# Optimization experiments

Hardware: AMD Instinct MI355X
Metric: run time of the kernel (lower is better)

## Reference

```python
import jax, jax.numpy as jnp
import numpy as np
from functools import partial

B, T, H, W, CIN, F = 8, 16, 64, 64, 32, 32
K = 3
BN_EPS = 1e-3


def _conv(x, w):
    # x: [N,H,W,Cin], w: [kh,kw,Cin,Cout], SAME padding, stride 1
    return jax.lax.conv_general_dilated(
        x, w, window_strides=(1, 1), padding='SAME',
        dimension_numbers=('NHWC', 'HWIO', 'NHWC'))


def _hard_sigmoid(x):
    # Keras hard_sigmoid: clip(0.2*x + 0.5, 0, 1)
    return jnp.clip(0.2 * x + 0.5, 0.0, 1.0)


def setup_inputs() -> dict:
    key = jax.random.key(0)
    ks = jax.random.split(key, 4)
    x = jax.random.normal(ks[0], (B, T, H, W, CIN), dtype=jnp.float32)
    Wx = jax.random.normal(ks[1], (K, K, CIN, 4 * F), dtype=jnp.float32) * 0.05
    Wh = jax.random.normal(ks[2], (K, K, F, 4 * F), dtype=jnp.float32) * 0.05
    b = jnp.zeros((4 * F,), dtype=jnp.float32)
    gamma = jnp.ones((F,), dtype=jnp.float32)
    beta = jnp.zeros((F,), dtype=jnp.float32)
    moving_mean = jnp.zeros((F,), dtype=jnp.float32)
    moving_var = jnp.ones((F,), dtype=jnp.float32)
    return {"x": x, "Wx": Wx, "Wh": Wh, "b": b, "gamma": gamma,
            "beta": beta, "moving_mean": moving_mean, "moving_var": moving_var}


def _conv_lstm(x, Wx, Wh, b):
    # Precompute input-to-gate convs for all timesteps at once: [B*T,H,W,4F]
    xg = _conv(x.reshape(B * T, H, W, CIN), Wx) + b
    xg = xg.reshape(B, T, H, W, 4 * F).transpose(1, 0, 2, 3, 4)  # [T,B,H,W,4F]

    def step(carry, xg_t):
        h, c = carry
        g = xg_t + _conv(h, Wh)  # [B,H,W,4F]
        i, f, cc, o = jnp.split(g, 4, axis=-1)  # Keras gate order i,f,c,o
        i = _hard_sigmoid(i)
        f = _hard_sigmoid(f)
        o = _hard_sigmoid(o)
        c = f * c + i * jnp.tanh(cc)
        h = o * jnp.tanh(c)
        return (h, c), h

    h0 = jnp.zeros((B, H, W, F), dtype=x.dtype)
    c0 = jnp.zeros((B, H, W, F), dtype=x.dtype)
    _, hs = jax.lax.scan(step, (h0, c0), xg)  # hs: [T,B,H,W,F]
    return hs.transpose(1, 0, 2, 3, 4)  # [B,T,H,W,F]


def reference(x, Wx, Wh, b, gamma, beta, moving_mean, moving_var):
    y = _conv_lstm(x, Wx, Wh, b)
    # BatchNorm in inference mode (training=False): use moving stats, eps=1e-3
    inv = gamma * jax.lax.rsqrt(moving_var + BN_EPS)
    return y * inv + (beta - moving_mean * inv)
```

## Files before the change

### kernel.cpp

```cpp
#include <hip/hip_runtime.h>
#include <math.h>

#define PSTR 40
#define GSTR 35
#define GPL  (64 * GSTR)

typedef _Float16 half8 __attribute__((ext_vector_type(8)));
typedef float    f32x4 __attribute__((ext_vector_type(4)));

__device__ __forceinline__ float fast_tanh(float v) {
    float e = __expf(2.f * v);
    return 1.f - 2.f / (e + 1.f);
}
__device__ __forceinline__ float hsig(float v) {
    return fminf(fmaxf(0.2f * v + 0.5f, 0.f), 1.f);
}

__global__ void prep_w(const float* __restrict__ Wx, const float* __restrict__ Wh,
                       _Float16* __restrict__ Wcx, _Float16* __restrict__ Wch) {
    const int k = blockIdx.x;
    const int n = threadIdx.x;
    const int tap = k >> 6, ci = k & 63;
    if (ci < 32) Wcx[(tap * 128 + n) * 32 + ci]        = (_Float16)Wx[(tap * 32 + ci) * 128 + n];
    else         Wch[(tap * 128 + n) * 32 + (ci - 32)] = (_Float16)Wh[(tap * 32 + (ci - 32)) * 128 + n];
}

__global__ __launch_bounds__(256, 2)
void lstm_step_k(const float* __restrict__ x, const _Float16* __restrict__ Wcx,
                 const _Float16* __restrict__ Wch, const float* __restrict__ bias,
                 const float* __restrict__ gamma_, const float* __restrict__ beta_,
                 const float* __restrict__ mmean, const float* __restrict__ mvar,
                 const _Float16* __restrict__ hprev, _Float16* __restrict__ hnext,
                 float* __restrict__ csw, float* __restrict__ out, int t)
{
    __shared__ _Float16 xp[100 * PSTR];
    __shared__ _Float16 hp[100 * PSTR];
    __shared__ float    glds[4 * GPL];

    const int tid  = threadIdx.x;
    const int lane = tid & 63;
    const int w    = tid >> 6;
    const int l15  = lane & 15, quad = lane >> 4;
    const int b = blockIdx.x, tx = blockIdx.y, ty = blockIdx.z;
    const int px0 = tx * 8, py0 = ty * 8;
    const int tile = ty * 8 + tx;

    const float* xt = x + (((size_t)b * 16 + t) * 4096) * 32;
    for (int i = tid; i < 400; i += 256) {
        const int pos = i >> 2, q = i & 3;
        const int row = pos / 10, col = pos - row * 10;
        const int gy = py0 + row - 1, gx = px0 + col - 1;
        half8 hv = {0, 0, 0, 0, 0, 0, 0, 0};
        if ((unsigned)gy < 64u && (unsigned)gx < 64u) {
            const float* s = xt + ((size_t)(gy * 64 + gx)) * 32 + q * 8;
            const float4 v0 = *(const float4*)s;
            const float4 v1 = *(const float4*)(s + 4);
            hv = (half8){(_Float16)v0.x, (_Float16)v0.y, (_Float16)v0.z, (_Float16)v0.w,
                         (_Float16)v1.x, (_Float16)v1.y, (_Float16)v1.z, (_Float16)v1.w};
        }
        *(half8*)&xp[pos * PSTR + q * 8] = hv;
    }
    if (t > 0) {
        const _Float16* hb = hprev + (size_t)b * 4096 * 32;
        for (int i = tid; i < 400; i += 256) {
            const int pos = i >> 2, q = i & 3;
            const int row = pos / 10, col = pos - row * 10;
            const int gy = py0 + row - 1, gx = px0 + col - 1;
            half8 hv = {0, 0, 0, 0, 0, 0, 0, 0};
            if ((unsigned)gy < 64u && (unsigned)gx < 64u)
                hv = *(const half8*)(hb + ((size_t)(gy * 64 + gx)) * 32 + q * 8);
            *(half8*)&hp[pos * PSTR + q * 8] = hv;
        }
    }

    const float bi0 = bias[w * 32 + l15];
    const float bi1 = bias[w * 32 + 16 + l15];

    __syncthreads();

    f32x4 acc[4][2];
    #pragma unroll
    for (int mt = 0; mt < 4; ++mt) {
        acc[mt][0] = (f32x4){bi0, bi0, bi0, bi0};
        acc[mt][1] = (f32x4){bi1, bi1, bi1, bi1};
    }

    int pb[4];
    #pragma unroll
    for (int mt = 0; mt < 4; ++mt) {
        const int p = mt * 16 + l15;
        pb[mt] = ((mt * 2 + (l15 >> 3)) * 10 + (l15 & 7)) * PSTR + quad * 8;
    }
    const _Float16* wbx = Wcx + ((size_t)(w * 32 + l15)) * 32 + quad * 8;
    const _Float16* wbh = Wch + ((size_t)(w * 32 + l15)) * 32 + quad * 8;

    #pragma unroll
    for (int tap = 0; tap < 9; ++tap) {
        const int ky = tap / 3, kx = tap - ky * 3;
        const int toff = (ky * 10 + kx) * PSTR;
        half8 a[4];
        #pragma unroll
        for (int mt = 0; mt < 4; ++mt) a[mt] = *(const half8*)&xp[pb[mt] + toff];
        #pragma unroll
        for (int ntl = 0; ntl < 2; ++ntl) {
            const half8 bf = *(const half8*)(wbx + tap * 4096 + ntl * 512);
            #pragma unroll
            for (int mt = 0; mt < 4; ++mt)
                acc[mt][ntl] = __builtin_amdgcn_mfma_f32_16x16x32_f16(a[mt], bf, acc[mt][ntl], 0, 0, 0);
        }
    }
    if (t > 0) {
        #pragma unroll
        for (int tap = 0; tap < 9; ++tap) {
            const int ky = tap / 3, kx = tap - ky * 3;
            const int toff = (ky * 10 + kx) * PSTR;
            half8 a[4];
            #pragma unroll
            for (int mt = 0; mt < 4; ++mt) a[mt] = *(const half8*)&hp[pb[mt] + toff];
            #pragma unroll
            for (int ntl = 0; ntl < 2; ++ntl) {
                const half8 bf = *(const half8*)(wbh + tap * 4096 + ntl * 512);
                #pragma unroll
                for (int mt = 0; mt < 4; ++mt)
                    acc[mt][ntl] = __builtin_amdgcn_mfma_f32_16x16x32_f16(a[mt], bf, acc[mt][ntl], 0, 0, 0);
            }
        }
    }

    #pragma unroll
    for (int mt = 0; mt < 4; ++mt)
        #pragma unroll
        for (int ntl = 0; ntl < 2; ++ntl)
            #pragma unroll
            for (int r = 0; r < 4; ++r) {
                const int px = mt * 16 + quad * 4 + r;
                glds[w * GPL + px * GSTR + ntl * 16 + l15] = acc[mt][ntl][r];
            }

    __syncthreads();

    const int pxt = tid >> 2, f0 = (tid & 3) * 8;
    const int gy = py0 + (pxt >> 3), gx = px0 + (pxt & 7);

    float gav[8], bev[8], mmv[8], mvv[8];
    *(float4*)&gav[0] = *(const float4*)&gamma_[f0];
    *(float4*)&gav[4] = *(const float4*)&gamma_[f0 + 4];
    *(float4*)&bev[0] = *(const float4*)&beta_[f0];
    *(float4*)&bev[4] = *(const float4*)&beta_[f0 + 4];
    *(float4*)&mmv[0] = *(const float4*)&mmean[f0];
    *(float4*)&mmv[4] = *(const float4*)&mmean[f0 + 4];
    *(float4*)&mvv[0] = *(const float4*)&mvar[f0];
    *(float4*)&mvv[4] = *(const float4*)&mvar[f0 + 4];

    float* cp = csw + (((size_t)b * 64 + tile) * 256 + tid) * 8;
    float cov[8];
    #pragma unroll
    for (int j = 0; j < 8; ++j) cov[j] = 0.f;
    if (t > 0) {
        *(f32x4*)&cov[0] = *(const f32x4*)cp;
        *(f32x4*)&cov[4] = *(const f32x4*)(cp + 4);
    }

    const int gb = pxt * GSTR + f0;
    half8 hv8;
    float ov[8], cnv[8];
    #pragma unroll
    for (int j = 0; j < 8; ++j) {
        const float gi = glds[0 * GPL + gb + j];
        const float gf = glds[1 * GPL + gb + j];
        const float gc = glds[2 * GPL + gb + j];
        const float go = glds[3 * GPL + gb + j];
        const float inv = gav[j] * rsqrtf(mvv[j] + 1e-3f);
        const float bnb = bev[j] - mmv[j] * inv;
        const float cn = hsig(gf) * cov[j] + hsig(gi) * fast_tanh(gc);
        const float hh = hsig(go) * fast_tanh(cn);
        cnv[j] = cn;
        hv8[j] = (_Float16)hh;
        ov[j] = hh * inv + bnb;
    }

    const size_t pix = ((size_t)(gy * 64 + gx)) * 32 + f0;
    _Float16* hq = hnext + (size_t)b * 4096 * 32;
    float* oq = out + (((size_t)b * 16 + t) * 4096) * 32;
    *(half8*)(hq + pix) = hv8;
    *(float4*)(oq + pix)     = *(float4*)&ov[0];
    *(float4*)(oq + pix + 4) = *(float4*)&ov[4];
    *(f32x4*)cp       = *(f32x4*)&cnv[0];
    *(f32x4*)(cp + 4) = *(f32x4*)&cnv[4];
}

extern "C" void kernel_launch(void* const* d_in, const int* in_sizes, int n_in,
                              void* d_out, int out_size, void* d_ws, size_t ws_size,
                              hipStream_t stream)
{
    const float* x      = (const float*)d_in[0];
    const float* Wx     = (const float*)d_in[1];
    const float* Wh     = (const float*)d_in[2];
    const float* bias   = (const float*)d_in[3];
    const float* gamma_ = (const float*)d_in[4];
    const float* beta_  = (const float*)d_in[5];
    const float* mmean  = (const float*)d_in[6];
    const float* mvar   = (const float*)d_in[7];
    float* out = (float*)d_out;

    char* wsb = (char*)d_ws;
    _Float16* h0  = (_Float16*)(wsb);
    _Float16* h1  = (_Float16*)(wsb + (1 << 21));
    float*    csw = (float*)(wsb + (1 << 22));
    _Float16* Wcx = (_Float16*)(wsb + (1 << 23));
    _Float16* Wch = (_Float16*)(wsb + (1 << 23) + 73728);

    prep_w<<<dim3(576), dim3(128), 0, stream>>>(Wx, Wh, Wcx, Wch);

    _Float16* hpr = h0;
    _Float16* hnx = h1;
    for (int t = 0; t < 16; ++t) {
        lstm_step_k<<<dim3(8, 8, 8), 256, 0, stream>>>(
            x, Wcx, Wch, bias, gamma_, beta_, mmean, mvar, hpr, hnx, csw, out, t);
        _Float16* tmp = hpr; hpr = hnx; hnx = tmp;
    }
}
```

Baseline: 293.0 us.

## Halve spatial tile to 8x4 pixels, doubling grid blocks per LSTM step

Shrinks each block's output tile from 8x8 to 8x4 pixels, so the grid per timestep doubles to 1024 blocks. LDS use per block drops and launch bounds rise to 4 blocks per CU, which gives more parallelism and occupancy to hide the latency of each short step launch. It also drops the h and c stores on the last timestep and swaps the divide-by-10 for a multiply-shift. In exchange, the 3x3 halo now costs more redundant loads per output pixel, and each wave issues fewer MFMAs per weight fragment it loads.

```diff
diff --git a/kernel.cpp b/kernel.cpp
--- a/kernel.cpp
+++ b/kernel.cpp
@@ -1,11 +1,12 @@
 #include <hip/hip_runtime.h>
 #include <math.h>
 
-#define PSTR 40
-#define GSTR 35
-#define GPL  (64 * GSTR)
+#define PSTR  40
+#define GSTR  35
+#define GPL32 (32 * GSTR)
 
 typedef _Float16 half8 __attribute__((ext_vector_type(8)));
+typedef _Float16 half4 __attribute__((ext_vector_type(4)));
 typedef float    f32x4 __attribute__((ext_vector_type(4)));
 
 __device__ __forceinline__ float fast_tanh(float v) {
@@ -15,6 +16,7 @@
 __device__ __forceinline__ float hsig(float v) {
     return fminf(fmaxf(0.2f * v + 0.5f, 0.f), 1.f);
 }
+__device__ __forceinline__ int div10(int p) { return (p * 205) >> 11; }
 
 __global__ void prep_w(const float* __restrict__ Wx, const float* __restrict__ Wh,
                        _Float16* __restrict__ Wcx, _Float16* __restrict__ Wch) {
@@ -25,7 +27,7 @@
     else         Wch[(tap * 128 + n) * 32 + (ci - 32)] = (_Float16)Wh[(tap * 32 + (ci - 32)) * 128 + n];
 }
 
-__global__ __launch_bounds__(256, 2)
+__global__ __launch_bounds__(256, 4)
 void lstm_step_k(const float* __restrict__ x, const _Float16* __restrict__ Wcx,
                  const _Float16* __restrict__ Wch, const float* __restrict__ bias,
                  const float* __restrict__ gamma_, const float* __restrict__ beta_,
@@ -33,22 +35,22 @@
                  const _Float16* __restrict__ hprev, _Float16* __restrict__ hnext,
                  float* __restrict__ csw, float* __restrict__ out, int t)
 {
-    __shared__ _Float16 xp[100 * PSTR];
-    __shared__ _Float16 hp[100 * PSTR];
-    __shared__ float    glds[4 * GPL];
+    __shared__ _Float16 xp[60 * PSTR];
+    __shared__ _Float16 hp[60 * PSTR];
+    __shared__ float    glds[4 * GPL32];
 
     const int tid  = threadIdx.x;
     const int lane = tid & 63;
     const int w    = tid >> 6;
     const int l15  = lane & 15, quad = lane >> 4;
     const int b = blockIdx.x, tx = blockIdx.y, ty = blockIdx.z;
-    const int px0 = tx * 8, py0 = ty * 8;
+    const int px0 = tx * 8, py0 = ty * 4;
     const int tile = ty * 8 + tx;
 
     const float* xt = x + (((size_t)b * 16 + t) * 4096) * 32;
-    for (int i = tid; i < 400; i += 256) {
-        const int pos = i >> 2, q = i & 3;
-        const int row = pos / 10, col = pos - row * 10;
+    if (tid < 240) {
+        const int cell = tid >> 2, q = tid & 3;
+        const int row = div10(cell), col = cell - row * 10;
         const int gy = py0 + row - 1, gx = px0 + col - 1;
         half8 hv = {0, 0, 0, 0, 0, 0, 0, 0};
         if ((unsigned)gy < 64u && (unsigned)gx < 64u) {
@@ -58,19 +60,17 @@
             hv = (half8){(_Float16)v0.x, (_Float16)v0.y, (_Float16)v0.z, (_Float16)v0.w,
                          (_Float16)v1.x, (_Float16)v1.y, (_Float16)v1.z, (_Float16)v1.w};
         }
-        *(half8*)&xp[pos * PSTR + q * 8] = hv;
-    }
-    if (t > 0) {
+        *(half8*)&xp[cell * PSTR + q * 8] = hv;
+    }
+    if (t > 0 && tid < 240) {
         const _Float16* hb = hprev + (size_t)b * 4096 * 32;
-        for (int i = tid; i < 400; i += 256) {
-            const int pos = i >> 2, q = i & 3;
-            const int row = pos / 10, col = pos - row * 10;
-            const int gy = py0 + row - 1, gx = px0 + col - 1;
-            half8 hv = {0, 0, 0, 0, 0, 0, 0, 0};
-            if ((unsigned)gy < 64u && (unsigned)gx < 64u)
-                hv = *(const half8*)(hb + ((size_t)(gy * 64 + gx)) * 32 + q * 8);
-            *(half8*)&hp[pos * PSTR + q * 8] = hv;
-        }
+        const int cell = tid >> 2, q = tid & 3;
+        const int row = div10(cell), col = cell - row * 10;
+        const int gy = py0 + row - 1, gx = px0 + col - 1;
+        half8 hv = {0, 0, 0, 0, 0, 0, 0, 0};
+        if ((unsigned)gy < 64u && (unsigned)gx < 64u)
+            hv = *(const half8*)(hb + ((size_t)(gy * 64 + gx)) * 32 + q * 8);
+        *(half8*)&hp[cell * PSTR + q * 8] = hv;
     }
 
     const float bi0 = bias[w * 32 + l15];
@@ -78,19 +78,17 @@
 
     __syncthreads();
 
-    f32x4 acc[4][2];
-    #pragma unroll
-    for (int mt = 0; mt < 4; ++mt) {
-        acc[mt][0] = (f32x4){bi0, bi0, bi0, bi0};
-        acc[mt][1] = (f32x4){bi1, bi1, bi1, bi1};
-    }
-
-    int pb[4];
-    #pragma unroll
-    for (int mt = 0; mt < 4; ++mt) {
-        const int p = mt * 16 + l15;
+    f32x4 acc[2][2];
+    acc[0][0] = (f32x4){bi0, bi0, bi0, bi0};
+    acc[0][1] = (f32x4){bi1, bi1, bi1, bi1};
+    acc[1][0] = acc[0][0];
+    acc[1][1] = acc[0][1];
+
+    int pb[2];
+    #pragma unroll
+    for (int mt = 0; mt < 2; ++mt)
         pb[mt] = ((mt * 2 + (l15 >> 3)) * 10 + (l15 & 7)) * PSTR + quad * 8;
-    }
+
     const _Float16* wbx = Wcx + ((size_t)(w * 32 + l15)) * 32 + quad * 8;
     const _Float16* wbh = Wch + ((size_t)(w * 32 + l15)) * 32 + quad * 8;
 
@@ -98,15 +96,13 @@
     for (int tap = 0; tap < 9; ++tap) {
         const int ky = tap / 3, kx = tap - ky * 3;
         const int toff = (ky * 10 + kx) * PSTR;
-        half8 a[4];
-        #pragma unroll
-        for (int mt = 0; mt < 4; ++mt) a[mt] = *(const half8*)&xp[pb[mt] + toff];
+        const half8 a0 = *(const half8*)&xp[pb[0] + toff];
+        const half8 a1 = *(const half8*)&xp[pb[1] + toff];
         #pragma unroll
         for (int ntl = 0; ntl < 2; ++ntl) {
             const half8 bf = *(const half8*)(wbx + tap * 4096 + ntl * 512);
-            #pragma unroll
-            for (int mt = 0; mt < 4; ++mt)
-                acc[mt][ntl] = __builtin_amdgcn_mfma_f32_16x16x32_f16(a[mt], bf, acc[mt][ntl], 0, 0, 0);
+            acc[0][ntl] = __builtin_amdgcn_mfma_f32_16x16x32_f16(a0, bf, acc[0][ntl], 0, 0, 0);
+            acc[1][ntl] = __builtin_amdgcn_mfma_f32_16x16x32_f16(a1, bf, acc[1][ntl], 0, 0, 0);
         }
     }
     if (t > 0) {
@@ -114,79 +110,69 @@
         for (int tap = 0; tap < 9; ++tap) {
             const int ky = tap / 3, kx = tap - ky * 3;
             const int toff = (ky * 10 + kx) * PSTR;
-            half8 a[4];
-            #pragma unroll
-            for (int mt = 0; mt < 4; ++mt) a[mt] = *(const half8*)&hp[pb[mt] + toff];
+            const half8 a0 = *(const half8*)&hp[pb[0] + toff];
+            const half8 a1 = *(const half8*)&hp[pb[1] + toff];
             #pragma unroll
             for (int ntl = 0; ntl < 2; ++ntl) {
                 const half8 bf = *(const half8*)(wbh + tap * 4096 + ntl * 512);
-                #pragma unroll
-                for (int mt = 0; mt < 4; ++mt)
-                    acc[mt][ntl] = __builtin_amdgcn_mfma_f32_16x16x32_f16(a[mt], bf, acc[mt][ntl], 0, 0, 0);
+                acc[0][ntl] = __builtin_amdgcn_mfma_f32_16x16x32_f16(a0, bf, acc[0][ntl], 0, 0, 0);
+                acc[1][ntl] = __builtin_amdgcn_mfma_f32_16x16x32_f16(a1, bf, acc[1][ntl], 0, 0, 0);
             }
         }
     }
 
     #pragma unroll
-    for (int mt = 0; mt < 4; ++mt)
+    for (int mt = 0; mt < 2; ++mt)
         #pragma unroll
         for (int ntl = 0; ntl < 2; ++ntl)
             #pragma unroll
             for (int r = 0; r < 4; ++r) {
                 const int px = mt * 16 + quad * 4 + r;
-                glds[w * GPL + px * GSTR + ntl * 16 + l15] = acc[mt][ntl][r];
+                glds[w * GPL32 + px * GSTR + ntl * 16 + l15] = acc[mt][ntl][r];
             }
 
     __syncthreads();
 
-    const int pxt = tid >> 2, f0 = (tid & 3) * 8;
+    const int pxt = tid >> 3, f0 = (tid & 7) * 4;
     const int gy = py0 + (pxt >> 3), gx = px0 + (pxt & 7);
 
-    float gav[8], bev[8], mmv[8], mvv[8];
-    *(float4*)&gav[0] = *(const float4*)&gamma_[f0];
-    *(float4*)&gav[4] = *(const float4*)&gamma_[f0 + 4];
-    *(float4*)&bev[0] = *(const float4*)&beta_[f0];
-    *(float4*)&bev[4] = *(const float4*)&beta_[f0 + 4];
-    *(float4*)&mmv[0] = *(const float4*)&mmean[f0];
-    *(float4*)&mmv[4] = *(const float4*)&mmean[f0 + 4];
-    *(float4*)&mvv[0] = *(const float4*)&mvar[f0];
-    *(float4*)&mvv[4] = *(const float4*)&mvar[f0 + 4];
-
-    float* cp = csw + (((size_t)b * 64 + tile) * 256 + tid) * 8;
-    float cov[8];
-    #pragma unroll
-    for (int j = 0; j < 8; ++j) cov[j] = 0.f;
-    if (t > 0) {
-        *(f32x4*)&cov[0] = *(const f32x4*)cp;
-        *(f32x4*)&cov[4] = *(const f32x4*)(cp + 4);
-    }
+    const float4 gav = *(const float4*)&gamma_[f0];
+    const float4 bev = *(const float4*)&beta_[f0];
+    const float4 mmv = *(const float4*)&mmean[f0];
+    const float4 mvv = *(const float4*)&mvar[f0];
+
+    float* cp = csw + (((size_t)b * 128 + tile) * 256 + tid) * 4;
+    f32x4 cov = (f32x4){0.f, 0.f, 0.f, 0.f};
+    if (t > 0) cov = *(const f32x4*)cp;
 
     const int gb = pxt * GSTR + f0;
-    half8 hv8;
-    float ov[8], cnv[8];
-    #pragma unroll
-    for (int j = 0; j < 8; ++j) {
-        const float gi = glds[0 * GPL + gb + j];
-        const float gf = glds[1 * GPL + gb + j];
-        const float gc = glds[2 * GPL + gb + j];
-        const float go = glds[3 * GPL + gb + j];
-        const float inv = gav[j] * rsqrtf(mvv[j] + 1e-3f);
-        const float bnb = bev[j] - mmv[j] * inv;
+    half4 hv4;
+    f32x4 ov, cnv;
+    #pragma unroll
+    for (int j = 0; j < 4; ++j) {
+        const float gi = glds[0 * GPL32 + gb + j];
+        const float gf = glds[1 * GPL32 + gb + j];
+        const float gc = glds[2 * GPL32 + gb + j];
+        const float go = glds[3 * GPL32 + gb + j];
+        const float ga = ((const float*)&gav)[j];
+        const float mv = ((const float*)&mvv)[j];
+        const float inv = ga * rsqrtf(mv + 1e-3f);
+        const float bnb = ((const float*)&bev)[j] - ((const float*)&mmv)[j] * inv;
         const float cn = hsig(gf) * cov[j] + hsig(gi) * fast_tanh(gc);
         const float hh = hsig(go) * fast_tanh(cn);
         cnv[j] = cn;
-        hv8[j] = (_Float16)hh;
+        hv4[j] = (_Float16)hh;
         ov[j] = hh * inv + bnb;
     }
 
     const size_t pix = ((size_t)(gy * 64 + gx)) * 32 + f0;
-    _Float16* hq = hnext + (size_t)b * 4096 * 32;
     float* oq = out + (((size_t)b * 16 + t) * 4096) * 32;
-    *(half8*)(hq + pix) = hv8;
-    *(float4*)(oq + pix)     = *(float4*)&ov[0];
-    *(float4*)(oq + pix + 4) = *(float4*)&ov[4];
-    *(f32x4*)cp       = *(f32x4*)&cnv[0];
-    *(f32x4*)(cp + 4) = *(f32x4*)&cnv[4];
+    *(float4*)(oq + pix) = *(float4*)&ov;
+    if (t < 15) {
+        _Float16* hq = hnext + (size_t)b * 4096 * 32;
+        *(half4*)(hq + pix) = hv4;
+        *(f32x4*)cp = cnv;
+    }
 }
 
 extern "C" void kernel_launch(void* const* d_in, const int* in_sizes, int n_in,
@@ -215,7 +201,7 @@
     _Float16* hpr = h0;
     _Float16* hnx = h1;
     for (int t = 0; t < 16; ++t) {
-        lstm_step_k<<<dim3(8, 8, 8), 256, 0, stream>>>(
+        lstm_step_k<<<dim3(8, 8, 16), 256, 0, stream>>>(
             x, Wcx, Wch, bias, gamma_, beta_, mmean, mvar, hpr, hnx, csw, out, t);
         _Float16* tmp = hpr; hpr = hnx; hnx = tmp;
     }
```

Measured after the change: 328.5 us. +12.1%, slower.

## Hoist input-to-gate convolution out of recurrent loop into one batched kernel

Applied to the files above, without the earlier changes.

Moves the x-to-gate convolution into a separate kernel that runs over all B*T frames in a single launch. Its fp16 gate preactivations (bias included) are stored in the MFMA register layout, so each step kernel only loads them and runs the recurrent h convolution. This shortens the serial per-step critical path and gives the x conv a much wider grid. In exchange it adds a large fp16 intermediate buffer round trip through global memory, plus extra fp16 rounding of the preactivations. It also skips writing h and c on the last step.

```diff
diff --git a/kernel.cpp b/kernel.cpp
--- a/kernel.cpp
+++ b/kernel.cpp
@@ -25,27 +25,21 @@
     else         Wch[(tap * 128 + n) * 32 + (ci - 32)] = (_Float16)Wh[(tap * 32 + (ci - 32)) * 128 + n];
 }
 
-__global__ __launch_bounds__(256, 2)
-void lstm_step_k(const float* __restrict__ x, const _Float16* __restrict__ Wcx,
-                 const _Float16* __restrict__ Wch, const float* __restrict__ bias,
-                 const float* __restrict__ gamma_, const float* __restrict__ beta_,
-                 const float* __restrict__ mmean, const float* __restrict__ mvar,
-                 const _Float16* __restrict__ hprev, _Float16* __restrict__ hnext,
-                 float* __restrict__ csw, float* __restrict__ out, int t)
+__global__ __launch_bounds__(256, 4)
+void xgemm(const float* __restrict__ x, const _Float16* __restrict__ Wcx,
+           const float* __restrict__ bias, _Float16* __restrict__ xg)
 {
     __shared__ _Float16 xp[100 * PSTR];
-    __shared__ _Float16 hp[100 * PSTR];
-    __shared__ float    glds[4 * GPL];
 
     const int tid  = threadIdx.x;
     const int lane = tid & 63;
     const int w    = tid >> 6;
     const int l15  = lane & 15, quad = lane >> 4;
-    const int b = blockIdx.x, tx = blockIdx.y, ty = blockIdx.z;
+    const int tx = blockIdx.x, ty = blockIdx.y, z = blockIdx.z;
     const int px0 = tx * 8, py0 = ty * 8;
     const int tile = ty * 8 + tx;
 
-    const float* xt = x + (((size_t)b * 16 + t) * 4096) * 32;
+    const float* xt = x + ((size_t)z * 4096) * 32;
     for (int i = tid; i < 400; i += 256) {
         const int pos = i >> 2, q = i & 3;
         const int row = pos / 10, col = pos - row * 10;
@@ -60,6 +54,70 @@
         }
         *(half8*)&xp[pos * PSTR + q * 8] = hv;
     }
+
+    const float bi0 = bias[w * 32 + l15];
+    const float bi1 = bias[w * 32 + 16 + l15];
+
+    __syncthreads();
+
+    f32x4 acc[4][2];
+    #pragma unroll
+    for (int mt = 0; mt < 4; ++mt) {
+        acc[mt][0] = (f32x4){bi0, bi0, bi0, bi0};
+        acc[mt][1] = (f32x4){bi1, bi1, bi1, bi1};
+    }
+
+    int pb[4];
+    #pragma unroll
+    for (int mt = 0; mt < 4; ++mt)
+        pb[mt] = ((mt * 2 + (l15 >> 3)) * 10 + (l15 & 7)) * PSTR + quad * 8;
+
+    const _Float16* wbx = Wcx + ((size_t)(w * 32 + l15)) * 32 + quad * 8;
+
+    #pragma unroll
+    for (int tap = 0; tap < 9; ++tap) {
+        const int ky = tap / 3, kx = tap - ky * 3;
+        const int toff = (ky * 10 + kx) * PSTR;
+        half8 a[4];
+        #pragma unroll
+        for (int mt = 0; mt < 4; ++mt) a[mt] = *(const half8*)&xp[pb[mt] + toff];
+        #pragma unroll
+        for (int ntl = 0; ntl < 2; ++ntl) {
+            const half8 bf = *(const half8*)(wbx + tap * 4096 + ntl * 512);
+            #pragma unroll
+            for (int mt = 0; mt < 4; ++mt)
+                acc[mt][ntl] = __builtin_amdgcn_mfma_f32_16x16x32_f16(a[mt], bf, acc[mt][ntl], 0, 0, 0);
+        }
+    }
+
+    _Float16* dst = xg + (((size_t)z * 64 + tile) * 256 + tid) * 32;
+    #pragma unroll
+    for (int mt = 0; mt < 4; ++mt) {
+        half8 o;
+        #pragma unroll
+        for (int r = 0; r < 4; ++r) { o[r] = (_Float16)acc[mt][0][r]; o[4 + r] = (_Float16)acc[mt][1][r]; }
+        *(half8*)(dst + mt * 8) = o;
+    }
+}
+
+__global__ __launch_bounds__(256, 2)
+void hstep(const _Float16* __restrict__ xg, const _Float16* __restrict__ Wch,
+           const float* __restrict__ gamma_, const float* __restrict__ beta_,
+           const float* __restrict__ mmean, const float* __restrict__ mvar,
+           const _Float16* __restrict__ hprev, _Float16* __restrict__ hnext,
+           float* __restrict__ csw, float* __restrict__ out, int t)
+{
+    __shared__ _Float16 hp[100 * PSTR];
+    __shared__ float    glds[4 * GPL];
+
+    const int tid  = threadIdx.x;
+    const int lane = tid & 63;
+    const int w    = tid >> 6;
+    const int l15  = lane & 15, quad = lane >> 4;
+    const int b = blockIdx.x, tx = blockIdx.y, ty = blockIdx.z;
+    const int px0 = tx * 8, py0 = ty * 8;
+    const int tile = ty * 8 + tx;
+
     if (t > 0) {
         const _Float16* hb = hprev + (size_t)b * 4096 * 32;
         for (int i = tid; i < 400; i += 256) {
@@ -73,43 +131,28 @@
         }
     }
 
-    const float bi0 = bias[w * 32 + l15];
-    const float bi1 = bias[w * 32 + 16 + l15];
+    const _Float16* xgp = xg + (((size_t)(b * 16 + t) * 64 + tile) * 256 + tid) * 32;
+    half8 xv[4];
+    #pragma unroll
+    for (int mt = 0; mt < 4; ++mt) xv[mt] = *(const half8*)(xgp + mt * 8);
 
     __syncthreads();
 
     f32x4 acc[4][2];
     #pragma unroll
-    for (int mt = 0; mt < 4; ++mt) {
-        acc[mt][0] = (f32x4){bi0, bi0, bi0, bi0};
-        acc[mt][1] = (f32x4){bi1, bi1, bi1, bi1};
-    }
-
-    int pb[4];
-    #pragma unroll
-    for (int mt = 0; mt < 4; ++mt) {
-        const int p = mt * 16 + l15;
-        pb[mt] = ((mt * 2 + (l15 >> 3)) * 10 + (l15 & 7)) * PSTR + quad * 8;
-    }
-    const _Float16* wbx = Wcx + ((size_t)(w * 32 + l15)) * 32 + quad * 8;
-    const _Float16* wbh = Wch + ((size_t)(w * 32 + l15)) * 32 + quad * 8;
-
-    #pragma unroll
-    for (int tap = 0; tap < 9; ++tap) {
-        const int ky = tap / 3, kx = tap - ky * 3;
-        const int toff = (ky * 10 + kx) * PSTR;
-        half8 a[4];
-        #pragma unroll
-        for (int mt = 0; mt < 4; ++mt) a[mt] = *(const half8*)&xp[pb[mt] + toff];
-        #pragma unroll
-        for (int ntl = 0; ntl < 2; ++ntl) {
-            const half8 bf = *(const half8*)(wbx + tap * 4096 + ntl * 512);
-            #pragma unroll
-            for (int mt = 0; mt < 4; ++mt)
-                acc[mt][ntl] = __builtin_amdgcn_mfma_f32_16x16x32_f16(a[mt], bf, acc[mt][ntl], 0, 0, 0);
-        }
-    }
+    for (int mt = 0; mt < 4; ++mt)
+        #pragma unroll
+        for (int ntl = 0; ntl < 2; ++ntl)
+            #pragma unroll
+            for (int r = 0; r < 4; ++r)
+                acc[mt][ntl][r] = (float)xv[mt][ntl * 4 + r];
+
     if (t > 0) {
+        int pb[4];
+        #pragma unroll
+        for (int mt = 0; mt < 4; ++mt)
+            pb[mt] = ((mt * 2 + (l15 >> 3)) * 10 + (l15 & 7)) * PSTR + quad * 8;
+        const _Float16* wbh = Wch + ((size_t)(w * 32 + l15)) * 32 + quad * 8;
         #pragma unroll
         for (int tap = 0; tap < 9; ++tap) {
             const int ky = tap / 3, kx = tap - ky * 3;
@@ -180,13 +223,15 @@
     }
 
     const size_t pix = ((size_t)(gy * 64 + gx)) * 32 + f0;
-    _Float16* hq = hnext + (size_t)b * 4096 * 32;
     float* oq = out + (((size_t)b * 16 + t) * 4096) * 32;
-    *(half8*)(hq + pix) = hv8;
     *(float4*)(oq + pix)     = *(float4*)&ov[0];
     *(float4*)(oq + pix + 4) = *(float4*)&ov[4];
-    *(f32x4*)cp       = *(f32x4*)&cnv[0];
-    *(f32x4*)(cp + 4) = *(f32x4*)&cnv[4];
+    if (t < 15) {
+        _Float16* hq = hnext + (size_t)b * 4096 * 32;
+        *(half8*)(hq + pix) = hv8;
+        *(f32x4*)cp       = *(f32x4*)&cnv[0];
+        *(f32x4*)(cp + 4) = *(f32x4*)&cnv[4];
+    }
 }
 
 extern "C" void kernel_launch(void* const* d_in, const int* in_sizes, int n_in,
@@ -207,16 +252,19 @@
     _Float16* h0  = (_Float16*)(wsb);
     _Float16* h1  = (_Float16*)(wsb + (1 << 21));
     float*    csw = (float*)(wsb + (1 << 22));
-    _Float16* Wcx = (_Float16*)(wsb + (1 << 23));
-    _Float16* Wch = (_Float16*)(wsb + (1 << 23) + 73728);
+    _Float16* xg  = (_Float16*)(wsb + (1 << 23));
+    _Float16* Wcx = (_Float16*)(wsb + (1 << 23) + (1 << 27));
+    _Float16* Wch = (_Float16*)(wsb + (1 << 23) + (1 << 27) + 73728);
 
     prep_w<<<dim3(576), dim3(128), 0, stream>>>(Wx, Wh, Wcx, Wch);
+
+    xgemm<<<dim3(8, 8, 128), 256, 0, stream>>>(x, Wcx, bias, xg);
 
     _Float16* hpr = h0;
     _Float16* hnx = h1;
     for (int t = 0; t < 16; ++t) {
-        lstm_step_k<<<dim3(8, 8, 8), 256, 0, stream>>>(
-            x, Wcx, Wch, bias, gamma_, beta_, mmean, mvar, hpr, hnx, csw, out, t);
+        hstep<<<dim3(8, 8, 8), 256, 0, stream>>>(
+            xg, Wch, gamma_, beta_, mmean, mvar, hpr, hnx, csw, out, t);
         _Float16* tmp = hpr; hpr = hnx; hnx = tmp;
     }
 }
```

Measured after the change: 338.3 us. 1.15x slower.

## Widen spatial tile to 16x8 with 512-thread blocks and skip last-step state writes

Applied to the files above, without the earlier changes.

Each block now covers a 16x8 pixel tile with 8 waves, four gate groups times two row groups, instead of an 8x8 tile with 4 waves. The halo overhead per pixel shrinks (18x10 loaded for 128 pixels versus 10x10 for 64), and the grid is halved. The gate LDS stride changes to 33, a division by 18 is replaced with a multiply-shift, and the final timestep no longer writes h and c state. Fewer blocks (256) with larger LDS use may reduce occupancy and latency hiding across the 256 CUs.

```diff
diff --git a/kernel.cpp b/kernel.cpp
--- a/kernel.cpp
+++ b/kernel.cpp
@@ -2,8 +2,8 @@
 #include <math.h>
 
 #define PSTR 40
-#define GSTR 35
-#define GPL  (64 * GSTR)
+#define GSTR 33
+#define GPL  (128 * GSTR)
 
 typedef _Float16 half8 __attribute__((ext_vector_type(8)));
 typedef float    f32x4 __attribute__((ext_vector_type(4)));
@@ -15,6 +15,7 @@
 __device__ __forceinline__ float hsig(float v) {
     return fminf(fmaxf(0.2f * v + 0.5f, 0.f), 1.f);
 }
+__device__ __forceinline__ int div18(int c) { return (c * 57) >> 10; }
 
 __global__ void prep_w(const float* __restrict__ Wx, const float* __restrict__ Wh,
                        _Float16* __restrict__ Wcx, _Float16* __restrict__ Wch) {
@@ -25,7 +26,7 @@
     else         Wch[(tap * 128 + n) * 32 + (ci - 32)] = (_Float16)Wh[(tap * 32 + (ci - 32)) * 128 + n];
 }
 
-__global__ __launch_bounds__(256, 2)
+__global__ __launch_bounds__(512, 2)
 void lstm_step_k(const float* __restrict__ x, const _Float16* __restrict__ Wcx,
                  const _Float16* __restrict__ Wch, const float* __restrict__ bias,
                  const float* __restrict__ gamma_, const float* __restrict__ beta_,
@@ -33,22 +34,23 @@
                  const _Float16* __restrict__ hprev, _Float16* __restrict__ hnext,
                  float* __restrict__ csw, float* __restrict__ out, int t)
 {
-    __shared__ _Float16 xp[100 * PSTR];
-    __shared__ _Float16 hp[100 * PSTR];
+    __shared__ _Float16 xp[180 * PSTR];
+    __shared__ _Float16 hp[180 * PSTR];
     __shared__ float    glds[4 * GPL];
 
     const int tid  = threadIdx.x;
     const int lane = tid & 63;
     const int w    = tid >> 6;
     const int l15  = lane & 15, quad = lane >> 4;
+    const int g    = w & 3, mtg = w >> 2;
     const int b = blockIdx.x, tx = blockIdx.y, ty = blockIdx.z;
-    const int px0 = tx * 8, py0 = ty * 8;
-    const int tile = ty * 8 + tx;
+    const int px0 = tx * 16, py0 = ty * 8;
+    const int tile = ty * 4 + tx;
 
     const float* xt = x + (((size_t)b * 16 + t) * 4096) * 32;
-    for (int i = tid; i < 400; i += 256) {
-        const int pos = i >> 2, q = i & 3;
-        const int row = pos / 10, col = pos - row * 10;
+    for (int i = tid; i < 720; i += 512) {
+        const int cell = i >> 2, q = i & 3;
+        const int row = div18(cell), col = cell - row * 18;
         const int gy = py0 + row - 1, gx = px0 + col - 1;
         half8 hv = {0, 0, 0, 0, 0, 0, 0, 0};
         if ((unsigned)gy < 64u && (unsigned)gx < 64u) {
@@ -58,89 +60,88 @@
             hv = (half8){(_Float16)v0.x, (_Float16)v0.y, (_Float16)v0.z, (_Float16)v0.w,
                          (_Float16)v1.x, (_Float16)v1.y, (_Float16)v1.z, (_Float16)v1.w};
         }
-        *(half8*)&xp[pos * PSTR + q * 8] = hv;
+        *(half8*)&xp[cell * PSTR + q * 8] = hv;
     }
     if (t > 0) {
         const _Float16* hb = hprev + (size_t)b * 4096 * 32;
-        for (int i = tid; i < 400; i += 256) {
-            const int pos = i >> 2, q = i & 3;
-            const int row = pos / 10, col = pos - row * 10;
+        for (int i = tid; i < 720; i += 512) {
+            const int cell = i >> 2, q = i & 3;
+            const int row = div18(cell), col = cell - row * 18;
             const int gy = py0 + row - 1, gx = px0 + col - 1;
             half8 hv = {0, 0, 0, 0, 0, 0, 0, 0};
             if ((unsigned)gy < 64u && (unsigned)gx < 64u)
                 hv = *(const half8*)(hb + ((size_t)(gy * 64 + gx)) * 32 + q * 8);
-            *(half8*)&hp[pos * PSTR + q * 8] = hv;
-        }
-    }
-
-    const float bi0 = bias[w * 32 + l15];
-    const float bi1 = bias[w * 32 + 16 + l15];
+            *(half8*)&hp[cell * PSTR + q * 8] = hv;
+        }
+    }
+
+    const float bi0 = bias[g * 32 + l15];
+    const float bi1 = bias[g * 32 + 16 + l15];
 
     __syncthreads();
 
     f32x4 acc[4][2];
     #pragma unroll
-    for (int mt = 0; mt < 4; ++mt) {
-        acc[mt][0] = (f32x4){bi0, bi0, bi0, bi0};
-        acc[mt][1] = (f32x4){bi1, bi1, bi1, bi1};
+    for (int mi = 0; mi < 4; ++mi) {
+        acc[mi][0] = (f32x4){bi0, bi0, bi0, bi0};
+        acc[mi][1] = (f32x4){bi1, bi1, bi1, bi1};
     }
 
     int pb[4];
     #pragma unroll
-    for (int mt = 0; mt < 4; ++mt) {
-        const int p = mt * 16 + l15;
-        pb[mt] = ((mt * 2 + (l15 >> 3)) * 10 + (l15 & 7)) * PSTR + quad * 8;
-    }
-    const _Float16* wbx = Wcx + ((size_t)(w * 32 + l15)) * 32 + quad * 8;
-    const _Float16* wbh = Wch + ((size_t)(w * 32 + l15)) * 32 + quad * 8;
+    for (int mi = 0; mi < 4; ++mi)
+        pb[mi] = ((mtg * 4 + mi) * 18 + l15) * PSTR + quad * 8;
+
+    const _Float16* wbx = Wcx + ((size_t)(g * 32 + l15)) * 32 + quad * 8;
+    const _Float16* wbh = Wch + ((size_t)(g * 32 + l15)) * 32 + quad * 8;
 
     #pragma unroll
     for (int tap = 0; tap < 9; ++tap) {
         const int ky = tap / 3, kx = tap - ky * 3;
-        const int toff = (ky * 10 + kx) * PSTR;
+        const int toff = (ky * 18 + kx) * PSTR;
         half8 a[4];
         #pragma unroll
-        for (int mt = 0; mt < 4; ++mt) a[mt] = *(const half8*)&xp[pb[mt] + toff];
+        for (int mi = 0; mi < 4; ++mi) a[mi] = *(const half8*)&xp[pb[mi] + toff];
         #pragma unroll
         for (int ntl = 0; ntl < 2; ++ntl) {
             const half8 bf = *(const half8*)(wbx + tap * 4096 + ntl * 512);
             #pragma unroll
-            for (int mt = 0; mt < 4; ++mt)
-                acc[mt][ntl] = __builtin_amdgcn_mfma_f32_16x16x32_f16(a[mt], bf, acc[mt][ntl], 0, 0, 0);
+            for (int mi = 0; mi < 4; ++mi)
+                acc[mi][ntl] = __builtin_amdgcn_mfma_f32_16x16x32_f16(a[mi], bf, acc[mi][ntl], 0, 0, 0);
         }
     }
     if (t > 0) {
         #pragma unroll
         for (int tap = 0; tap < 9; ++tap) {
             const int ky = tap / 3, kx = tap - ky * 3;
-            const int toff = (ky * 10 + kx) * PSTR;
+            const int toff = (ky * 18 + kx) * PSTR;
             half8 a[4];
             #pragma unroll
-            for (int mt = 0; mt < 4; ++mt) a[mt] = *(const half8*)&hp[pb[mt] + toff];
+            for (int mi = 0; mi < 4; ++mi) a[mi] = *(const half8*)&hp[pb[mi] + toff];
             #pragma unroll
             for (int ntl = 0; ntl < 2; ++ntl) {
                 const half8 bf = *(const half8*)(wbh + tap * 4096 + ntl * 512);
                 #pragma unroll
-                for (int mt = 0; mt < 4; ++mt)
-                    acc[mt][ntl] = __builtin_amdgcn_mfma_f32_16x16x32_f16(a[mt], bf, acc[mt][ntl], 0, 0, 0);
+                for (int mi = 0; mi < 4; ++mi)
+                    acc[mi][ntl] = __builtin_amdgcn_mfma_f32_16x16x32_f16(a[mi], bf, acc[mi][ntl], 0, 0, 0);
             }
         }
     }
 
     #pragma unroll
-    for (int mt = 0; mt < 4; ++mt)
+    for (int mi = 0; mi < 4; ++mi)
         #pragma unroll
         for (int ntl = 0; ntl < 2; ++ntl)
             #pragma unroll
             for (int r = 0; r < 4; ++r) {
-                const int px = mt * 16 + quad * 4 + r;
-                glds[w * GPL + px * GSTR + ntl * 16 + l15] = acc[mt][ntl][r];
+                const int px = (mtg * 4 + mi) * 16 + quad * 4 + r;
+                glds[g * GPL + px * GSTR + ntl * 16 + l15] = acc[mi][ntl][r];
             }
 
     __syncthreads();
 
     const int pxt = tid >> 2, f0 = (tid & 3) * 8;
-    const int gy = py0 + (pxt >> 3), gx = px0 + (pxt & 7);
+    const int gy = py0 + (pxt >> 4), gx = px0 + (pxt & 15);
 
     float gav[8], bev[8], mmv[8], mvv[8];
     *(float4*)&gav[0] = *(const float4*)&gamma_[f0];
@@ -152,7 +153,7 @@
     *(float4*)&mvv[0] = *(const float4*)&mvar[f0];
     *(float4*)&mvv[4] = *(const float4*)&mvar[f0 + 4];
 
-    float* cp = csw + (((size_t)b * 64 + tile) * 256 + tid) * 8;
+    float* cp = csw + (((size_t)b * 32 + tile) * 512 + tid) * 8;
     float cov[8];
     #pragma unroll
     for (int j = 0; j < 8; ++j) cov[j] = 0.f;
@@ -180,13 +181,15 @@
     }
 
     const size_t pix = ((size_t)(gy * 64 + gx)) * 32 + f0;
-    _Float16* hq = hnext + (size_t)b * 4096 * 32;
     float* oq = out + (((size_t)b * 16 + t) * 4096) * 32;
-    *(half8*)(hq + pix) = hv8;
     *(float4*)(oq + pix)     = *(float4*)&ov[0];
     *(float4*)(oq + pix + 4) = *(float4*)&ov[4];
-    *(f32x4*)cp       = *(f32x4*)&cnv[0];
-    *(f32x4*)(cp + 4) = *(f32x4*)&cnv[4];
+    if (t < 15) {
+        _Float16* hq = hnext + (size_t)b * 4096 * 32;
+        *(half8*)(hq + pix) = hv8;
+        *(f32x4*)cp       = *(f32x4*)&cnv[0];
+        *(f32x4*)(cp + 4) = *(f32x4*)&cnv[4];
+    }
 }
 
 extern "C" void kernel_launch(void* const* d_in, const int* in_sizes, int n_in,
@@ -215,7 +218,7 @@
     _Float16* hpr = h0;
     _Float16* hnx = h1;
     for (int t = 0; t < 16; ++t) {
-        lstm_step_k<<<dim3(8, 8, 8), 256, 0, stream>>>(
+        lstm_step_k<<<dim3(8, 4, 8), 512, 0, stream>>>(
             x, Wcx, Wch, bias, gamma_, beta_, mmean, mvar, hpr, hnx, csw, out, t);
         _Float16* tmp = hpr; hpr = hnx; hnx = tmp;
     }
```

New measurement: 295.9 us. Within noise of the previous version (+1.0%).
